# Performance work log

Measured on AMD Instinct MI355X. Metric: run time of the kernel, lower is better.

The kernel has to match this reference:

```python
import jax, jax.numpy as jnp
import numpy as np

K = 8            # kernel volume = down_ratio^3 = 2^3
N_IN = 40000     # coarse (input) active voxels
N_OUT = 150000   # fine (output/skip) active voxels
C_IN = 128
C_EMB = 128
C_SKIP = 128
EPS = 1e-5


def setup_inputs() -> dict:
    key = jax.random.key(0)
    ks = jax.random.split(key, 8)
    x_feat = jax.random.normal(ks[0], (N_IN, C_IN), dtype=jnp.float32)
    skip_feat = jax.random.normal(ks[1], (N_OUT, C_SKIP), dtype=jnp.float32)
    pair_in = jax.random.randint(ks[2], (K, N_OUT), 0, N_IN, dtype=jnp.int32)
    pair_out = jax.random.randint(ks[3], (K, N_OUT), 0, N_OUT, dtype=jnp.int32)
    W_up = jax.random.normal(ks[4], (K, C_IN, C_EMB), dtype=jnp.float32) * 0.02
    W1 = jax.random.normal(ks[5], (C_SKIP + C_EMB, C_EMB), dtype=jnp.float32) * 0.05
    W2 = jax.random.normal(ks[6], (C_EMB, C_EMB), dtype=jnp.float32) * 0.05
    return {
        "x_feat": x_feat, "skip_feat": skip_feat,
        "pair_in": pair_in, "pair_out": pair_out,
        "W_up": W_up,
        "g0": jnp.ones((C_EMB,), jnp.float32), "b0": jnp.zeros((C_EMB,), jnp.float32),
        "W1": W1, "b1": jnp.zeros((C_EMB,), jnp.float32),
        "g1": jnp.ones((C_EMB,), jnp.float32), "be1": jnp.zeros((C_EMB,), jnp.float32),
        "W2": W2, "b2": jnp.zeros((C_EMB,), jnp.float32),
        "g2": jnp.ones((C_EMB,), jnp.float32), "be2": jnp.zeros((C_EMB,), jnp.float32),
    }


def _bn(x, gamma, beta):
    # BatchNorm1d over the point axis (training-mode batch stats, biased var)
    m = jnp.mean(x, axis=0)
    v = jnp.mean(jnp.square(x - m), axis=0)
    return (x - m) * jax.lax.rsqrt(v + EPS) * gamma + beta


def reference(x_feat, skip_feat, pair_in, pair_out, W_up,
              g0, b0, W1, b1, g1, be1, W2, b2, g2, be2):
    n_out = skip_feat.shape[0]
    # SparseInverseConv3d: gather coarse features, per-offset GEMM, scatter-add
    out = jnp.zeros((n_out, W_up.shape[2]), dtype=x_feat.dtype)
    for k in range(K):  # fixed small kernel volume, structurally distinct weights
        contrib = x_feat[pair_in[k]] @ W_up[k]          # [P, C_emb]
        out = out.at[pair_out[k]].add(contrib)
    up = jax.nn.relu(_bn(out, g0, b0))                  # [N_out, C_emb]

    # fuse: concat([up, skip]) -> Linear/BN/ReLU x2, residual with up
    h = jnp.concatenate([up, skip_feat], axis=1)        # [N_out, C_emb+C_skip]
    h = jax.nn.relu(_bn(h @ W1 + b1, g1, be1))
    h = jax.nn.relu(_bn(h @ W2 + b2, g2, be2))
    return h + up
```

## Files before the change

### kernel.cpp

```cpp
#include <hip/hip_runtime.h>

#define KVOL 8
#define NIN 40000
#define NOUT 150000
#define C 128
#define EPSV 1e-5f
#define NPAIR (KVOL * NOUT)
#define GM ((NOUT + 63) / 64)
#define GM2 ((NOUT + 127) / 128)
#define GUP (NIN / 64)
#define NBUCK ((NOUT + 255) / 256)
#define NSTR 8
#define SCAP 768
#define BCAP 4096
#define GBUCK ((NPAIR + 4095) / 4096)

typedef __attribute__((ext_vector_type(8))) __bf16 bf16x8;
typedef __attribute__((ext_vector_type(4))) float f32x4;
typedef __attribute__((ext_vector_type(8))) unsigned short us8;

__device__ __forceinline__ unsigned short fbf(float f) {
    unsigned u = __float_as_uint(f);
    u += 0x7fffu + ((u >> 16) & 1u);
    return (unsigned short)(u >> 16);
}
__device__ __forceinline__ float bff(unsigned short s) {
    return __uint_as_float(((unsigned)s) << 16);
}

__global__ __launch_bounds__(256) void k_prep_w(
    const float* __restrict__ Wup, const float* __restrict__ W1, const float* __restrict__ W2,
    unsigned short* __restrict__ WT)
{
    int i = blockIdx.x * 256 + threadIdx.x;
    if (i < 11 * 16384) {
        int b = i >> 14, r = i & 16383;
        int k = r >> 7, n = r & 127;
        const float* src = (b < 8) ? (Wup + (size_t)b * 16384)
                         : (b < 10) ? (W1 + (size_t)(b - 8) * 16384) : W2;
        WT[(size_t)b * 16384 + n * 128 + k] = fbf(src[k * 128 + n]);
    }
}

__global__ __launch_bounds__(256) void k_up(
    const float* __restrict__ x, const unsigned short* __restrict__ WT,
    unsigned short* __restrict__ Y)
{
    __shared__ __align__(16) unsigned short Alds[64][136];
    __shared__ __align__(16) unsigned short Wlds[128][136];
    const int t = threadIdx.x;
    const int wave = t >> 6, lane = t & 63;
    const int l15 = lane & 15, lhi = lane >> 4;
    const int R = blockIdx.x * 64;
    const float4* A4 = (const float4*)x;
    #pragma unroll
    for (int j = 0; j < 8; ++j) {
        int idx = t + j * 256;
        int row = idx >> 5, c4 = idx & 31;
        int grow = R + row;
        float4 v = make_float4(0.f, 0.f, 0.f, 0.f);
        if (grow < NIN) v = A4[(size_t)grow * 32 + c4];
        ushort4 o;
        o.x = fbf(v.x); o.y = fbf(v.y); o.z = fbf(v.z); o.w = fbf(v.w);
        *(ushort4*)&Alds[row][c4 * 4] = o;
    }
    __syncthreads();
    bf16x8 af[4];
    #pragma unroll
    for (int kk = 0; kk < 4; ++kk)
        af[kk] = *(const bf16x8*)&Alds[wave * 16 + l15][kk * 32 + lhi * 8];
    for (int k = 0; k < KVOL; ++k) {
        __syncthreads();
        const us8* Wsrc = (const us8*)(WT + (size_t)k * C * C);
        #pragma unroll
        for (int j = 0; j < 8; ++j) {
            int slot = t + j * 256;
            int n = slot >> 4, koff = (slot & 15) * 8;
            *(us8*)&Wlds[n][koff] = Wsrc[slot];
        }
        __syncthreads();
        f32x4 acc[8];
        #pragma unroll
        for (int n = 0; n < 8; ++n) acc[n] = (f32x4){0.f, 0.f, 0.f, 0.f};
        #pragma unroll
        for (int n = 0; n < 8; ++n) {
            #pragma unroll
            for (int kk = 0; kk < 4; ++kk) {
                bf16x8 bfr = *(const bf16x8*)&Wlds[n * 16 + l15][kk * 32 + lhi * 8];
                acc[n] = __builtin_amdgcn_mfma_f32_16x16x32_bf16(af[kk], bfr, acc[n], 0, 0, 0);
            }
        }
        unsigned short* Yk = Y + (size_t)k * NIN * C;
        #pragma unroll
        for (int n = 0; n < 8; ++n) {
            const int col = n * 16 + l15;
            #pragma unroll
            for (int r = 0; r < 4; ++r) {
                int row = R + wave * 16 + lhi * 4 + r;
                if (row < NIN) Yk[(size_t)row * C + col] = fbf(acc[n][r]);
            }
        }
    }
}

template<int PHASES, bool BNIN, bool STATS>
__global__ __launch_bounds__(512) void k_mfma(
    const void* __restrict__ A0v, const void* __restrict__ A1v,
    const unsigned short* __restrict__ WT,
    const float* __restrict__ bias,
    unsigned short* __restrict__ outp, int M,
    const float* __restrict__ bn_stats, const float* __restrict__ bn_g, const float* __restrict__ bn_b,
    float* __restrict__ parts)
{
    __shared__ __align__(16) unsigned short Alds[128][136];
    __shared__ __align__(16) unsigned short Wlds[128][136];
    __shared__ float sscale[C], sshift[C];
    const int t = threadIdx.x;
    const int wave = t >> 6, lane = t & 63;
    const int l15 = lane & 15, lhi = lane >> 4;
    const int R = blockIdx.x * 128;

    if (BNIN) {
        if (t < C) {
            float m = bn_stats[t] * (1.0f / NOUT);
            float var = bn_stats[C + t] * (1.0f / NOUT) - m * m;
            float sc = bn_g[t] * rsqrtf(var + EPSV);
            sscale[t] = sc;
            sshift[t] = fmaf(-m, sc, bn_b[t]);
        }
        __syncthreads();
    }

    f32x4 acc[8];
    #pragma unroll
    for (int n = 0; n < 8; ++n) acc[n] = (f32x4){0.f, 0.f, 0.f, 0.f};

    {
        const us8* Wsrc = (const us8*)WT;
        #pragma unroll
        for (int j = 0; j < 4; ++j) {
            int slot = t + j * 512;
            *(us8*)&Wlds[slot >> 4][(slot & 15) * 8] = Wsrc[slot];
        }
        const us8* A8 = (const us8*)A0v;
        #pragma unroll
        for (int j = 0; j < 4; ++j) {
            int slot = t + j * 512;
            int row = slot >> 4, s15 = slot & 15, koff = s15 * 8;
            int grow = R + row;
            us8 v = (us8){0, 0, 0, 0, 0, 0, 0, 0};
            if (grow < M) v = A8[(size_t)grow * 16 + s15];
            if (BNIN) {
                us8 w;
                #pragma unroll
                for (int i = 0; i < 8; ++i) {
                    float f = fmaxf(fmaf(bff(v[i]), sscale[koff + i], sshift[koff + i]), 0.f);
                    w[i] = fbf(f);
                }
                v = w;
            }
            *(us8*)&Alds[row][koff] = v;
        }
    }
    __syncthreads();

    if constexpr (PHASES == 2) {
        us8 wreg[4];
        float4 areg[8];
        {
            const us8* Wsrc1 = (const us8*)(WT + C * C);
            #pragma unroll
            for (int j = 0; j < 4; ++j) wreg[j] = Wsrc1[t + j * 512];
            const float4* A41 = (const float4*)A1v;
            #pragma unroll
            for (int j = 0; j < 8; ++j) {
                int slot = t + j * 512;
                int row = slot >> 5, c4 = slot & 31;
                int grow = R + row;
                float4 v = make_float4(0.f, 0.f, 0.f, 0.f);
                if (grow < M) v = A41[(size_t)grow * 32 + c4];
                areg[j] = v;
            }
        }
        {
            bf16x8 af[4];
            #pragma unroll
            for (int kk = 0; kk < 4; ++kk)
                af[kk] = *(const bf16x8*)&Alds[wave * 16 + l15][kk * 32 + lhi * 8];
            #pragma unroll
            for (int n = 0; n < 8; ++n) {
                #pragma unroll
                for (int kk = 0; kk < 4; ++kk) {
                    bf16x8 bfr = *(const bf16x8*)&Wlds[n * 16 + l15][kk * 32 + lhi * 8];
                    acc[n] = __builtin_amdgcn_mfma_f32_16x16x32_bf16(af[kk], bfr, acc[n], 0, 0, 0);
                }
            }
        }
        __syncthreads();
        #pragma unroll
        for (int j = 0; j < 4; ++j) {
            int slot = t + j * 512;
            *(us8*)&Wlds[slot >> 4][(slot & 15) * 8] = wreg[j];
        }
        #pragma unroll
        for (int j = 0; j < 8; ++j) {
            int slot = t + j * 512;
            int row = slot >> 5, c4 = slot & 31;
            float4 v = areg[j];
            ushort4 o;
            o.x = fbf(v.x); o.y = fbf(v.y); o.z = fbf(v.z); o.w = fbf(v.w);
            *(ushort4*)&Alds[row][c4 * 4] = o;
        }
        __syncthreads();
    }
    {
        bf16x8 af[4];
        #pragma unroll
        for (int kk = 0; kk < 4; ++kk)
            af[kk] = *(const bf16x8*)&Alds[wave * 16 + l15][kk * 32 + lhi * 8];
        #pragma unroll
        for (int n = 0; n < 8; ++n) {
            #pragma unroll
            for (int kk = 0; kk < 4; ++kk) {
                bf16x8 bfr = *(const bf16x8*)&Wlds[n * 16 + l15][kk * 32 + lhi * 8];
                acc[n] = __builtin_amdgcn_mfma_f32_16x16x32_bf16(af[kk], bfr, acc[n], 0, 0, 0);
            }
        }
    }
    __syncthreads();

    float* sbS = (float*)&Alds[0][0];
    float* sbQ = sbS + 1024;
    #pragma unroll
    for (int n = 0; n < 8; ++n) {
        const int col = n * 16 + l15;
        float bv = bias[col];
        float s = 0.f, q = 0.f;
        #pragma unroll
        for (int r = 0; r < 4; ++r) {
            int row = R + wave * 16 + lhi * 4 + r;
            if (row < M) {
                float v = acc[n][r] + bv;
                outp[(size_t)row * C + col] = fbf(v);
                if (STATS) { s += v; q = fmaf(v, v, q); }
            }
        }
        if (STATS) {
            s += __shfl_xor(s, 16); s += __shfl_xor(s, 32);
            q += __shfl_xor(q, 16); q += __shfl_xor(q, 32);
            if (lane < 16) {
                sbS[wave * 128 + col] = s;
                sbQ[wave * 128 + col] = q;
            }
        }
    }
    if (STATS) {
        __syncthreads();
        if (t < 128) {
            float S = 0.f;
            #pragma unroll
            for (int w = 0; w < 8; ++w) S += sbS[w * 128 + t];
            parts[(size_t)blockIdx.x * 256 + t] = S;
        } else if (t < 256) {
            int cc = t - 128;
            float Q = 0.f;
            #pragma unroll
            for (int w = 0; w < 8; ++w) Q += sbQ[w * 128 + cc];
            parts[(size_t)blockIdx.x * 256 + t] = Q;
        }
    }
}

__global__ __launch_bounds__(256) void k_reduce(const float* __restrict__ parts, int nb,
                                                float* __restrict__ stats)
{
    const int t = threadIdx.x;
    float s0 = 0.f, s1 = 0.f, s2 = 0.f, s3 = 0.f;
    for (int b = blockIdx.x * 4; b < nb; b += gridDim.x * 4) {
        if (b < nb)     s0 += parts[(size_t)b * 256 + t];
        if (b + 1 < nb) s1 += parts[(size_t)(b + 1) * 256 + t];
        if (b + 2 < nb) s2 += parts[(size_t)(b + 2) * 256 + t];
        if (b + 3 < nb) s3 += parts[(size_t)(b + 3) * 256 + t];
    }
    atomicAdd(&stats[t], (s0 + s1) + (s2 + s3));
}

__global__ __launch_bounds__(256) void k_bucket2(
    const int* __restrict__ pout, const int* __restrict__ pin,
    int* __restrict__ bcnt, unsigned int* __restrict__ bbuf)
{
    __shared__ int cnt[NBUCK];
    __shared__ int base[NBUCK];
    __shared__ int run[NBUCK];
    const int t = threadIdx.x;
    const int str = blockIdx.x & (NSTR - 1);
    const int i0 = blockIdx.x * 4096;
    for (int b = t; b < NBUCK; b += 256) { cnt[b] = 0; run[b] = 0; }
    __syncthreads();
    for (int j = t; j < 4096; j += 256) {
        int i = i0 + j;
        if (i < NPAIR) atomicAdd(&cnt[pout[i] >> 8], 1);
    }
    __syncthreads();
    for (int b = t; b < NBUCK; b += 256) {
        int c = cnt[b];
        base[b] = c ? atomicAdd(&bcnt[str * NBUCK + b], c) : 0;
    }
    __syncthreads();
    for (int j = t; j < 4096; j += 256) {
        int i = i0 + j;
        if (i < NPAIR) {
            int o = pout[i];
            int k = i / NOUT;
            unsigned e = (unsigned)(k * NIN + pin[i]);
            int b = o >> 8;
            int dst = base[b] + atomicAdd(&run[b], 1);
            if (dst < SCAP)
                bbuf[((size_t)str * NBUCK + b) * SCAP + dst] = ((unsigned)(o & 255) << 24) | e;
        }
    }
}

__global__ __launch_bounds__(256) void k_sortgather(
    const int* __restrict__ bcnt, const unsigned int* __restrict__ bbuf,
    const us8* __restrict__ Y8, us8* __restrict__ up8, float* __restrict__ parts)
{
    __shared__ unsigned int pr[BCAP];
    __shared__ unsigned int srt[BCAP];
    __shared__ int cnt[256], sd[256], ofs2[256];
    const int t = threadIdx.x;
    const int b = blockIdx.x;
    int segbase = 0;
    #pragma unroll
    for (int s = 0; s < NSTR; ++s) {
        int ns = min(bcnt[s * NBUCK + b], SCAP);
        const unsigned int* g = bbuf + ((size_t)s * NBUCK + b) * SCAP;
        for (int j = t; j < ns; j += 256) pr[segbase + j] = g[j];
        segbase += ns;
    }
    const int n = segbase;
    cnt[t] = 0;
    __syncthreads();
    for (int j = t; j < n; j += 256) atomicAdd(&cnt[pr[j] >> 24], 1);
    __syncthreads();
    sd[t] = cnt[t];
    __syncthreads();
    for (int off = 1; off < 256; off <<= 1) {
        int a = sd[t];
        int bb = (t >= off) ? sd[t - off] : 0;
        __syncthreads();
        sd[t] = a + bb;
        __syncthreads();
    }
    ofs2[t] = sd[t] - cnt[t];
    __syncthreads();
    for (int j = t; j < n; j += 256) {
        unsigned p = pr[j];
        int pos = atomicAdd(&ofs2[p >> 24], 1);
        srt[pos] = p & 0xFFFFFFu;
    }
    __syncthreads();
    float* sS = (float*)pr;
    float* sQ = sS + 2048;
    const int rl = t >> 4, c8 = t & 15;
    float s8[8], q8[8];
    #pragma unroll
    for (int i = 0; i < 8; ++i) { s8[i] = 0.f; q8[i] = 0.f; }
    #pragma unroll
    for (int it = 0; it < 16; ++it) {
        int r = it * 16 + rl;
        int o = b * 256 + r;
        if (o < NOUT) {
            int j1 = sd[r], j0 = j1 - cnt[r];
            float a[8];
            #pragma unroll
            for (int i = 0; i < 8; ++i) a[i] = 0.f;
            int j = j0;
            for (; j + 1 < j1; j += 2) {
                unsigned e0 = srt[j], e1 = srt[j + 1];
                us8 u0 = Y8[(size_t)e0 * 16 + c8];
                us8 u1 = Y8[(size_t)e1 * 16 + c8];
                #pragma unroll
                for (int i = 0; i < 8; ++i) a[i] += bff(u0[i]) + bff(u1[i]);
            }
            if (j < j1) {
                unsigned e0 = srt[j];
                us8 u0 = Y8[(size_t)e0 * 16 + c8];
                #pragma unroll
                for (int i = 0; i < 8; ++i) a[i] += bff(u0[i]);
            }
            us8 o8;
            #pragma unroll
            for (int i = 0; i < 8; ++i) {
                o8[i] = fbf(a[i]);
                s8[i] += a[i];
                q8[i] = fmaf(a[i], a[i], q8[i]);
            }
            up8[(size_t)o * 16 + c8] = o8;
        }
    }
    #pragma unroll
    for (int i = 0; i < 8; ++i) {
        sS[(rl * 16 + c8) * 8 + i] = s8[i];
        sQ[(rl * 16 + c8) * 8 + i] = q8[i];
    }
    __syncthreads();
    if (t < 128) {
        const int cc = t >> 3, ii = t & 7;
        float S = 0.f, Q = 0.f;
        #pragma unroll
        for (int r = 0; r < 16; ++r) {
            S += sS[(r * 16 + cc) * 8 + ii];
            Q += sQ[(r * 16 + cc) * 8 + ii];
        }
        parts[(size_t)b * 256 + t] = S;
        parts[(size_t)b * 256 + 128 + t] = Q;
    }
}

__global__ __launch_bounds__(256) void k_final(
    const us8* __restrict__ h2, const us8* __restrict__ upr, float* __restrict__ out,
    const float* __restrict__ stats2, const float* __restrict__ g2, const float* __restrict__ be2,
    const float* __restrict__ stats0, const float* __restrict__ g0, const float* __restrict__ b0)
{
    __shared__ float sc2[C], sh2[C], sc0[C], sh0[C];
    const int t = threadIdx.x;
    if (t < C) {
        float m2 = stats2[t] * (1.0f / NOUT);
        float v2 = stats2[C + t] * (1.0f / NOUT) - m2 * m2;
        float c2 = g2[t] * rsqrtf(v2 + EPSV);
        sc2[t] = c2; sh2[t] = fmaf(-m2, c2, be2[t]);
        float m0 = stats0[t] * (1.0f / NOUT);
        float v0 = stats0[C + t] * (1.0f / NOUT) - m0 * m0;
        float c0 = g0[t] * rsqrtf(v0 + EPSV);
        sc0[t] = c0; sh0[t] = fmaf(-m0, c0, b0[t]);
    }
    __syncthreads();
    const int idx0 = blockIdx.x * 256 + t;
    const int c8 = idx0 & 15;
    float l2s[8], l2h[8], l0s[8], l0h[8];
    #pragma unroll
    for (int i = 0; i < 8; ++i) {
        l2s[i] = sc2[c8 * 8 + i]; l2h[i] = sh2[c8 * 8 + i];
        l0s[i] = sc0[c8 * 8 + i]; l0h[i] = sh0[c8 * 8 + i];
    }
    const int total = NOUT * 16;
    for (int idx = idx0; idx < total; idx += gridDim.x * 256) {
        us8 h = h2[idx];
        us8 u = upr[idx];
        float o[8];
        #pragma unroll
        for (int i = 0; i < 8; ++i) {
            o[i] = fmaxf(fmaf(bff(h[i]), l2s[i], l2h[i]), 0.f)
                 + fmaxf(fmaf(bff(u[i]), l0s[i], l0h[i]), 0.f);
        }
        float4* dst = (float4*)&out[(size_t)idx * 8];
        dst[0] = make_float4(o[0], o[1], o[2], o[3]);
        dst[1] = make_float4(o[4], o[5], o[6], o[7]);
    }
}

extern "C" void kernel_launch(void* const* d_in, const int* in_sizes, int n_in,
                              void* d_out, int out_size, void* d_ws, size_t ws_size,
                              hipStream_t stream)
{
    const float* x    = (const float*)d_in[0];
    const float* skip = (const float*)d_in[1];
    const int*   pin  = (const int*)d_in[2];
    const int*   pout = (const int*)d_in[3];
    const float* Wup  = (const float*)d_in[4];
    const float* g0   = (const float*)d_in[5];
    const float* b0   = (const float*)d_in[6];
    const float* W1   = (const float*)d_in[7];
    const float* b1   = (const float*)d_in[8];
    const float* g1   = (const float*)d_in[9];
    const float* be1  = (const float*)d_in[10];
    const float* W2   = (const float*)d_in[11];
    const float* b2   = (const float*)d_in[12];
    const float* g2   = (const float*)d_in[13];
    const float* be2  = (const float*)d_in[14];
    float* outp = (float*)d_out;

    char* base = (char*)d_ws;
    unsigned short* Y      = (unsigned short*)base;
    unsigned short* h1     = (unsigned short*)base;
    unsigned short* h2     = (unsigned short*)(base + 40960000);
    unsigned short* up_raw = (unsigned short*)(base + 81920000);
    char* p = base + 81920000 + 38400000;
    unsigned short* WT = (unsigned short*)p; p += (size_t)11 * 16384 * 2;
    unsigned int* bbuf = (unsigned int*)p;  p += (size_t)NSTR * NBUCK * SCAP * 4;
    int* bcnt      = (int*)p; p += (size_t)NSTR * NBUCK * 4;
    float* parts0  = (float*)p; p += (size_t)NBUCK * 256 * 4;
    float* parts1  = (float*)p; p += (size_t)GM * 256 * 4;
    float* parts2  = (float*)p; p += (size_t)GM * 256 * 4;
    float* stats   = (float*)p; p += 3 * 256 * 4;

    hipMemsetAsync(bcnt, 0, (size_t)NSTR * NBUCK * 4, stream);
    hipMemsetAsync(stats, 0, 3 * 256 * 4, stream);

    k_prep_w<<<(11 * 16384 + 255) / 256, 256, 0, stream>>>(Wup, W1, W2, WT);

    k_up<<<GUP, 256, 0, stream>>>(x, WT, Y);

    k_bucket2<<<GBUCK, 256, 0, stream>>>(pout, pin, bcnt, bbuf);

    k_sortgather<<<NBUCK, 256, 0, stream>>>(bcnt, bbuf, (const us8*)Y, (us8*)up_raw, parts0);
    k_reduce<<<16, 256, 0, stream>>>(parts0, NBUCK, stats);

    k_mfma<2, true, true><<<GM2, 512, 0, stream>>>(
        up_raw, skip, WT + (size_t)8 * 16384, b1, h1, NOUT, stats, g0, b0, parts1);
    k_reduce<<<16, 256, 0, stream>>>(parts1, GM2, stats + 256);

    k_mfma<1, true, true><<<GM2, 512, 0, stream>>>(
        h1, nullptr, WT + (size_t)10 * 16384, b2, h2, NOUT, stats + 256, g1, be1, parts2);
    k_reduce<<<16, 256, 0, stream>>>(parts2, GM2, stats + 512);

    k_final<<<1024, 256, 0, stream>>>((const us8*)h2, (const us8*)up_raw, outp,
        stats + 512, g2, be2, stats, g0, b0);
}
```

Measured before the change: 296.8 us.

## Merge bucketing into the up-GEMM launch and halve sort-gather bucket size

Folds the pair-bucketing kernel into the coarse up-projection GEMM launch. The first blocks of the combined grid do bucketing and the rest do the GEMM, so the two independent stages run concurrently and one launch is removed. Buckets shrink from 256 to 128 output rows with a smaller per-stream capacity. This roughly halves sort-gather shared memory and doubles its block count, aiming at better occupancy and load balance. The BN statistics reduction in sort-gather now uses wave shuffles before a small shared-memory pass. The tighter per-stream capacity of 256 carries a small overflow risk under skewed inputs.

Result: no change. 301.5 us (+1.6%).

```diff
diff --git a/kernel.cpp b/kernel.cpp
--- a/kernel.cpp
+++ b/kernel.cpp
@@ -9,11 +9,13 @@
 #define GM ((NOUT + 63) / 64)
 #define GM2 ((NOUT + 127) / 128)
 #define GUP (NIN / 64)
-#define NBUCK ((NOUT + 255) / 256)
+#define BROWS 128
+#define NBUCK ((NOUT + BROWS - 1) / BROWS)
 #define NSTR 8
-#define SCAP 768
-#define BCAP 4096
+#define SCAP 256
+#define BCAP (NSTR * SCAP)
 #define GBUCK ((NPAIR + 4095) / 4096)
+#define GUPB (GBUCK + GUP)
 
 typedef __attribute__((ext_vector_type(8))) __bf16 bf16x8;
 typedef __attribute__((ext_vector_type(4))) float f32x4;
@@ -42,16 +44,53 @@
     }
 }
 
-__global__ __launch_bounds__(256) void k_up(
+__global__ __launch_bounds__(256) void k_upb(
     const float* __restrict__ x, const unsigned short* __restrict__ WT,
-    unsigned short* __restrict__ Y)
+    unsigned short* __restrict__ Y,
+    const int* __restrict__ pout, const int* __restrict__ pin,
+    int* __restrict__ bcnt, unsigned int* __restrict__ bbuf)
 {
     __shared__ __align__(16) unsigned short Alds[64][136];
     __shared__ __align__(16) unsigned short Wlds[128][136];
     const int t = threadIdx.x;
+
+    if (blockIdx.x < GBUCK) {
+        int* cnt = (int*)&Alds[0][0];
+        int* bas = cnt + NBUCK;
+        int* run = bas + NBUCK;
+        const int bid = blockIdx.x;
+        const int str = bid & (NSTR - 1);
+        const int i0 = bid * 4096;
+        for (int b = t; b < NBUCK; b += 256) { cnt[b] = 0; run[b] = 0; }
+        __syncthreads();
+        for (int j = t; j < 4096; j += 256) {
+            int i = i0 + j;
+            if (i < NPAIR) atomicAdd(&cnt[pout[i] >> 7], 1);
+        }
+        __syncthreads();
+        for (int b = t; b < NBUCK; b += 256) {
+            int c = cnt[b];
+            bas[b] = c ? atomicAdd(&bcnt[str * NBUCK + b], c) : 0;
+        }
+        __syncthreads();
+        for (int j = t; j < 4096; j += 256) {
+            int i = i0 + j;
+            if (i < NPAIR) {
+                int o = pout[i];
+                int k = i / NOUT;
+                unsigned e = (unsigned)(k * NIN + pin[i]);
+                int b = o >> 7;
+                int dst = bas[b] + atomicAdd(&run[b], 1);
+                if (dst < SCAP)
+                    bbuf[((size_t)str * NBUCK + b) * SCAP + dst] = ((unsigned)(o & 127) << 24) | e;
+            }
+        }
+        return;
+    }
+
     const int wave = t >> 6, lane = t & 63;
     const int l15 = lane & 15, lhi = lane >> 4;
-    const int R = blockIdx.x * 64;
+    const int R = (blockIdx.x - GBUCK) * 64;
     const float4* A4 = (const float4*)x;
     #pragma unroll
     for (int j = 0; j < 8; ++j) {
@@ -285,49 +324,13 @@
     atomicAdd(&stats[t], (s0 + s1) + (s2 + s3));
 }
 
-__global__ __launch_bounds__(256) void k_bucket2(
-    const int* __restrict__ pout, const int* __restrict__ pin,
-    int* __restrict__ bcnt, unsigned int* __restrict__ bbuf)
-{
-    __shared__ int cnt[NBUCK];
-    __shared__ int base[NBUCK];
-    __shared__ int run[NBUCK];
-    const int t = threadIdx.x;
-    const int str = blockIdx.x & (NSTR - 1);
-    const int i0 = blockIdx.x * 4096;
-    for (int b = t; b < NBUCK; b += 256) { cnt[b] = 0; run[b] = 0; }
-    __syncthreads();
-    for (int j = t; j < 4096; j += 256) {
-        int i = i0 + j;
-        if (i < NPAIR) atomicAdd(&cnt[pout[i] >> 8], 1);
-    }
-    __syncthreads();
-    for (int b = t; b < NBUCK; b += 256) {
-        int c = cnt[b];
-        base[b] = c ? atomicAdd(&bcnt[str * NBUCK + b], c) : 0;
-    }
-    __syncthreads();
-    for (int j = t; j < 4096; j += 256) {
-        int i = i0 + j;
-        if (i < NPAIR) {
-            int o = pout[i];
-            int k = i / NOUT;
-            unsigned e = (unsigned)(k * NIN + pin[i]);
-            int b = o >> 8;
-            int dst = base[b] + atomicAdd(&run[b], 1);
-            if (dst < SCAP)
-                bbuf[((size_t)str * NBUCK + b) * SCAP + dst] = ((unsigned)(o & 255) << 24) | e;
-        }
-    }
-}
-
 __global__ __launch_bounds__(256) void k_sortgather(
     const int* __restrict__ bcnt, const unsigned int* __restrict__ bbuf,
     const us8* __restrict__ Y8, us8* __restrict__ up8, float* __restrict__ parts)
 {
     __shared__ unsigned int pr[BCAP];
     __shared__ unsigned int srt[BCAP];
-    __shared__ int cnt[256], sd[256], ofs2[256];
+    __shared__ int cnt[BROWS], sd[BROWS], ofs2[BROWS];
     const int t = threadIdx.x;
     const int b = blockIdx.x;
     int segbase = 0;
@@ -339,20 +342,20 @@
         segbase += ns;
     }
     const int n = segbase;
-    cnt[t] = 0;
+    if (t < BROWS) cnt[t] = 0;
     __syncthreads();
     for (int j = t; j < n; j += 256) atomicAdd(&cnt[pr[j] >> 24], 1);
     __syncthreads();
-    sd[t] = cnt[t];
-    __syncthreads();
-    for (int off = 1; off < 256; off <<= 1) {
-        int a = sd[t];
-        int bb = (t >= off) ? sd[t - off] : 0;
-        __syncthreads();
-        sd[t] = a + bb;
-        __syncthreads();
-    }
-    ofs2[t] = sd[t] - cnt[t];
+    if (t < BROWS) sd[t] = cnt[t];
+    __syncthreads();
+    for (int off = 1; off < BROWS; off <<= 1) {
+        int a = (t < BROWS) ? sd[t] : 0;
+        int bb = (t < BROWS && t >= off) ? sd[t - off] : 0;
+        __syncthreads();
+        if (t < BROWS) sd[t] = a + bb;
+        __syncthreads();
+    }
+    if (t < BROWS) ofs2[t] = sd[t] - cnt[t];
     __syncthreads();
     for (int j = t; j < n; j += 256) {
         unsigned p = pr[j];
@@ -360,16 +363,15 @@
         srt[pos] = p & 0xFFFFFFu;
     }
     __syncthreads();
-    float* sS = (float*)pr;
-    float* sQ = sS + 2048;
+    const int wave = t >> 6, lane = t & 63;
     const int rl = t >> 4, c8 = t & 15;
     float s8[8], q8[8];
     #pragma unroll
     for (int i = 0; i < 8; ++i) { s8[i] = 0.f; q8[i] = 0.f; }
     #pragma unroll
-    for (int it = 0; it < 16; ++it) {
+    for (int it = 0; it < 8; ++it) {
         int r = it * 16 + rl;
-        int o = b * 256 + r;
+        int o = b * BROWS + r;
         if (o < NOUT) {
             int j1 = sd[r], j0 = j1 - cnt[r];
             float a[8];
@@ -401,17 +403,26 @@
     }
     #pragma unroll
     for (int i = 0; i < 8; ++i) {
-        sS[(rl * 16 + c8) * 8 + i] = s8[i];
-        sQ[(rl * 16 + c8) * 8 + i] = q8[i];
+        s8[i] += __shfl_xor(s8[i], 16); s8[i] += __shfl_xor(s8[i], 32);
+        q8[i] += __shfl_xor(q8[i], 16); q8[i] += __shfl_xor(q8[i], 32);
+    }
+    float* sS = (float*)pr;
+    float* sQ = sS + 512;
+    if (lane < 16) {
+        #pragma unroll
+        for (int i = 0; i < 8; ++i) {
+            sS[(wave * 16 + c8) * 8 + i] = s8[i];
+            sQ[(wave * 16 + c8) * 8 + i] = q8[i];
+        }
     }
     __syncthreads();
     if (t < 128) {
         const int cc = t >> 3, ii = t & 7;
         float S = 0.f, Q = 0.f;
         #pragma unroll
-        for (int r = 0; r < 16; ++r) {
-            S += sS[(r * 16 + cc) * 8 + ii];
-            Q += sQ[(r * 16 + cc) * 8 + ii];
+        for (int w = 0; w < 4; ++w) {
+            S += sS[(w * 16 + cc) * 8 + ii];
+            Q += sQ[(w * 16 + cc) * 8 + ii];
         }
         parts[(size_t)b * 256 + t] = S;
         parts[(size_t)b * 256 + 128 + t] = Q;
@@ -500,9 +511,7 @@
 
     k_prep_w<<<(11 * 16384 + 255) / 256, 256, 0, stream>>>(Wup, W1, W2, WT);
 
-    k_up<<<GUP, 256, 0, stream>>>(x, WT, Y);
-
-    k_bucket2<<<GBUCK, 256, 0, stream>>>(pout, pin, bcnt, bbuf);
+    k_upb<<<GUPB, 256, 0, stream>>>(x, WT, Y, pout, pin, bcnt, bbuf);
 
     k_sortgather<<<NBUCK, 256, 0, stream>>>(bcnt, bbuf, (const us8*)Y, (us8*)up_raw, parts0);
     k_reduce<<<16, 256, 0, stream>>>(parts0, NBUCK, stats);
```
